# Optimization experiments

Hardware: AMD Instinct MI355X
Metric: run time of the kernel (lower is better)

The kernel has to match this reference:

```python
import jax, jax.numpy as jnp
import numpy as np

EPS = 1e-5

def convbn_relu(x, W, g, b, m, v):
    # 1x1 conv [O,C] on NCHW input, then inference-mode BN, then ReLU
    y = jnp.einsum('oc,bchw->bohw', W, x)
    scale = (g * jax.lax.rsqrt(v + EPS))[:, None, None]
    y = (y - m[:, None, None]) * scale + b[:, None, None]
    return jax.nn.relu(y)


def setup_inputs() -> dict:
    key = jax.random.key(0)
    ks = jax.random.split(key, 7)
    B, C, H, W = 2, 256, 96, 96
    L = 6  # psi1, psi2, phi1, phi2, f_down, f_up
    x = jax.random.normal(ks[0], (B, C, H, W), dtype=jnp.float32)
    f_k = jax.random.normal(ks[1], (B, C, H, W), dtype=jnp.float32)
    Ws = jax.random.normal(ks[2], (L, C, C), dtype=jnp.float32) * (1.0 / 16.0)
    gammas = jax.random.uniform(ks[3], (L, C), dtype=jnp.float32)
    betas = jax.random.normal(ks[4], (L, C), dtype=jnp.float32) * 0.1
    means = jax.random.normal(ks[5], (L, C), dtype=jnp.float32) * 0.1
    vars_ = jax.random.uniform(ks[6], (L, C), dtype=jnp.float32) + 0.5
    return {"x": x, "f_k": f_k, "Ws": Ws, "gammas": gammas, "betas": betas, "means": means, "vars_": vars_}


def reference(x, f_k, Ws, gammas, betas, means, vars_):
    B, C, H, W = x.shape
    K = Ws.shape[1]
    p = lambda i: (Ws[i], gammas[i], betas[i], means[i], vars_[i])
    # psi(x): two convbn+relu
    q = convbn_relu(convbn_relu(x, *p(0)), *p(1)).reshape(B, K, H * W)
    q = jnp.transpose(q, (0, 2, 1))                      # [B, N, K]
    # phi(f_k): two convbn+relu
    k = convbn_relu(convbn_relu(f_k, *p(2)), *p(3)).reshape(B, K, H * W)  # [B, K, N]
    # f_down(f_k)
    v = convbn_relu(f_k, *p(4)).reshape(B, K, H * W)
    v = jnp.transpose(v, (0, 2, 1))                      # [B, N, K]
    # attention WITHOUT 1/sqrt(d) scaling, as in the original
    sim = jnp.einsum('bnk,bkm->bnm', q, k)               # [B, N, N]
    sim = jax.nn.softmax(sim, axis=-1)
    ctx = jnp.einsum('bnm,bmk->bnk', sim, v)             # [B, N, K]
    ctx = jnp.transpose(ctx, (0, 2, 1)).reshape(B, K, H, W)
    # f_up
    return convbn_relu(ctx, *p(5))
```

## Files before the change

kernel.cpp:

```cpp
#include <hip/hip_runtime.h>
#include <hip/hip_bf16.h>

typedef __bf16 bf16;
typedef __bf16 bf16x8 __attribute__((ext_vector_type(8)));
typedef float floatx4 __attribute__((ext_vector_type(4)));
typedef float floatx16 __attribute__((ext_vector_type(16)));

#define MFMA_BF16(a, b, c) __builtin_amdgcn_mfma_f32_16x16x32_bf16((a), (b), (c), 0, 0, 0)
#define MFMA32(a, b, c) __builtin_amdgcn_mfma_f32_32x32x16_bf16((a), (b), (c), 0, 0, 0)

static constexpr int CH = 256;
static constexpr int NPIX = 9216;
static constexpr int MTOT = 2 * NPIX;
static constexpr int NQB2 = 144;

__device__ __forceinline__ void async16(void* lds, const void* g) {
  __builtin_amdgcn_global_load_lds(
      (const __attribute__((address_space(1))) void*)g,
      (__attribute__((address_space(3))) void*)lds, 16, 0, 0);
}

__device__ __forceinline__ unsigned cvtpk(float lo, float hi) {
  unsigned r;
  asm("v_cvt_pk_bf16_f32 %0, %1, %2" : "=v"(r) : "v"(lo), "v"(hi));
  return r;
}

__device__ __forceinline__ void plswap(unsigned& a, unsigned& b) {
  asm volatile("v_permlane32_swap_b32 %0, %1" : "+v"(a), "+v"(b));
}
__device__ __forceinline__ float xmax32(float v) {
  unsigned a = __builtin_bit_cast(unsigned, v), b = a;
  plswap(a, b);
  return fmaxf(__builtin_bit_cast(float, a), __builtin_bit_cast(float, b));
}
__device__ __forceinline__ float xsum32(float v) {
  unsigned a = __builtin_bit_cast(unsigned, v), b = a;
  plswap(a, b);
  return __builtin_bit_cast(float, a) + __builtin_bit_cast(float, b);
}

__global__ void split_transpose2(const float* __restrict__ xin, const float* __restrict__ fkin,
                                 bf16* __restrict__ ohx, bf16* __restrict__ olx,
                                 bf16* __restrict__ ohf, bf16* __restrict__ olf,
                                 const float* __restrict__ W,
                                 const float* __restrict__ g, const float* __restrict__ b,
                                 const float* __restrict__ m, const float* __restrict__ v,
                                 bf16* __restrict__ Wh, bf16* __restrict__ Wl,
                                 float* __restrict__ scale, float* __restrict__ bias) {
  __shared__ float t[64][65];
  int bid = blockIdx.x;
  int tid = threadIdx.x;

  {
    int i = bid * 256 + tid;
    if (i < 6 * CH * CH) {
      float wv = W[i];
      bf16 h = (bf16)wv;
      Wh[i] = h;
      Wl[i] = (bf16)(wv - (float)h);
    }
    if (i < 6 * CH) {
      float s = g[i] * rsqrtf(v[i] + 1e-5f);
      scale[i] = s;
      bias[i] = b[i] - m[i] * s;
    }
  }

  const float* in; bf16 *oh, *ol;
  if (bid >= 1152) { in = fkin; oh = ohf; ol = olf; bid -= 1152; }
  else             { in = xin;  oh = ohx; ol = olx; }
  int bb = bid / 576, rem = bid % 576;
  int ct = rem / 144, nt = rem % 144;
  int c0 = ct * 64, n0 = nt * 64;
  int cr = tid >> 4, nc = (tid & 15) * 4;
  for (int rr = 0; rr < 64; rr += 16) {
    int c = cr + rr;
    const float* p = in + ((size_t)(bb * CH + c0 + c) * NPIX) + n0 + nc;
    float4 val = *(const float4*)p;
    t[c][nc + 0] = val.x; t[c][nc + 1] = val.y;
    t[c][nc + 2] = val.z; t[c][nc + 3] = val.w;
  }
  __syncthreads();
  int n = tid >> 2, cb = (tid & 3) * 16;
  bf16 hb[16], lb[16];
#pragma unroll
  for (int j = 0; j < 16; j++) {
    float xv = t[cb + j][n];
    bf16 h = (bf16)xv;
    hb[j] = h;
    lb[j] = (bf16)(xv - (float)h);
  }
  size_t idx = (size_t)(bb * NPIX + n0 + n) * CH + c0 + cb;
  *(bf16x8*)&oh[idx]     = *(bf16x8*)&hb[0];
  *(bf16x8*)&oh[idx + 8] = *(bf16x8*)&hb[8];
  *(bf16x8*)&ol[idx]     = *(bf16x8*)&lb[0];
  *(bf16x8*)&ol[idx + 8] = *(bf16x8*)&lb[8];
}

struct ConvJob {
  const bf16 *Ah, *Al, *Bh, *Bl;
  const float *scale, *bias;
  bf16 *Yh, *Yl; float *Yf;
  int mode;
  int bid0;
};

__global__ __launch_bounds__(256, 3) void conv128(ConvJob j0, ConvJob j1, ConvJob j2) {
  __shared__ bf16 lds[4][8 * 512];
  int gbid = blockIdx.x;
  ConvJob j; int bid;
  if (gbid < 288)      { j = j0; bid = gbid; }
  else if (gbid < 576) { j = j1; bid = gbid - 288; }
  else                 { j = j2; bid = gbid - 576 + j2.bid0; }

  int tid = threadIdx.x;
  int w = tid >> 6, l = tid & 63;
  int q = l >> 4, c16 = l & 15;
  int m0 = (bid >> 1) * 128;
  int o0 = (bid & 1) * 128;

  const bf16* src = (w == 0) ? j.Ah : (w == 1) ? j.Al : (w == 2) ? j.Bh : j.Bl;
  int rowbase = (w < 2) ? m0 : o0;
  const bf16* gp = src + (size_t)(rowbase + c16) * CH + q * 8;
  bf16* ldst = &lds[w][0];

  const floatx4 zero4 = {0.f, 0.f, 0.f, 0.f};
  floatx4 acc[4][4];
#pragma unroll
  for (int i = 0; i < 4; i++)
#pragma unroll
    for (int jj = 0; jj < 4; jj++) acc[i][jj] = zero4;

  int mo16 = (w & 1) * 4, no16 = (w >> 1) * 4;

  for (int k0 = 0; k0 < CH; k0 += 32) {
#pragma unroll
    for (int f = 0; f < 8; f++)
      async16(ldst + f * 512, gp + (size_t)f * 16 * CH + k0);
    __syncthreads();

    bf16x8 ah[4], al[4], bh[4], bl[4];
#pragma unroll
    for (int i = 0; i < 4; i++) {
      ah[i] = *(const bf16x8*)&lds[0][(mo16 + i) * 512 + l * 8];
      al[i] = *(const bf16x8*)&lds[1][(mo16 + i) * 512 + l * 8];
      bh[i] = *(const bf16x8*)&lds[2][(no16 + i) * 512 + l * 8];
      bl[i] = *(const bf16x8*)&lds[3][(no16 + i) * 512 + l * 8];
    }
#pragma unroll
    for (int i = 0; i < 4; i++)
#pragma unroll
      for (int jj = 0; jj < 4; jj++) {
        acc[i][jj] = MFMA_BF16(ah[i], bh[jj], acc[i][jj]);
        acc[i][jj] = MFMA_BF16(ah[i], bl[jj], acc[i][jj]);
        acc[i][jj] = MFMA_BF16(al[i], bh[jj], acc[i][jj]);
      }
    __syncthreads();
  }

  int mo = (w & 1) * 64, no = (w >> 1) * 64;
  float sc[4], bs[4];
#pragma unroll
  for (int jj = 0; jj < 4; jj++) {
    int o = o0 + no + 16 * jj + c16;
    sc[jj] = j.scale[o];
    bs[jj] = j.bias[o];
  }

  if (j.mode == 3) {
    bf16* tile = &lds[0][0];
    int b2 = (m0 >= NPIX) ? 1 : 0;
    int nr0 = m0 - b2 * NPIX;
#pragma unroll
    for (int hc = 0; hc < 2; hc++) {
      __syncthreads();
      if ((w >> 1) == hc) {
#pragma unroll
        for (int i = 0; i < 4; i++)
#pragma unroll
          for (int jj = 0; jj < 4; jj++)
#pragma unroll
            for (int r = 0; r < 4; r++) {
              float y = acc[i][jj][r] * sc[jj] + bs[jj];
              y = fmaxf(y, 0.f);
              int chl = no + 16 * jj + c16 - hc * 64;
              int rowl = mo + 16 * i + 4 * q + r;
              tile[chl * 136 + rowl] = (bf16)y;
            }
      }
      __syncthreads();
      int chl = tid >> 2, rseg = (tid & 3) * 32;
      bf16* dst = j.Yh + ((size_t)(b2 * CH + o0 + hc * 64 + chl)) * NPIX + nr0 + rseg;
#pragma unroll
      for (int k = 0; k < 4; k++)
        *(bf16x8*)(dst + 8 * k) = *(bf16x8*)&tile[chl * 136 + rseg + 8 * k];
    }
    return;
  }

#pragma unroll
  for (int i = 0; i < 4; i++) {
    int nrow = m0 + mo + 16 * i + 4 * q;
#pragma unroll
    for (int jj = 0; jj < 4; jj++) {
      int o = o0 + no + 16 * jj + c16;
#pragma unroll
      for (int r = 0; r < 4; r++) {
        float y = acc[i][jj][r] * sc[jj] + bs[jj];
        y = fmaxf(y, 0.f);
        size_t idx = (size_t)(nrow + r) * CH + o;
        if (j.mode == 2) {
          j.Yf[idx] = y;
        } else if (j.mode == 1) {
          j.Yh[idx] = (bf16)y;
        } else {
          bf16 h = (bf16)y;
          j.Yh[idx] = h;
          j.Yl[idx] = (bf16)(y - (float)h);
        }
      }
    }
  }
}

__global__ __launch_bounds__(256, 4) void conv64(
    const bf16* __restrict__ Ah, const bf16* __restrict__ Al,
    const bf16* __restrict__ Bh, const bf16* __restrict__ Bl,
    const float* __restrict__ scale, const float* __restrict__ bias,
    float* __restrict__ Yf) {
  __shared__ bf16 lds[24 * 512];
  int tid = threadIdx.x;
  int w = tid >> 6, l = tid & 63;
  int q = l >> 4, c16 = l & 15;
  int m0 = (blockIdx.x >> 1) * 64;
  int o0 = (blockIdx.x & 1) * 128;

  const floatx4 zero4 = {0.f, 0.f, 0.f, 0.f};
  floatx4 acc[4][2];
#pragma unroll
  for (int i = 0; i < 4; i++) { acc[i][0] = zero4; acc[i][1] = zero4; }

  for (int k0 = 0; k0 < CH; k0 += 32) {
#pragma unroll
    for (int ff = 0; ff < 6; ff++) {
      int f = w * 6 + ff;
      const bf16* src; int rbase, fl;
      if (f < 4)       { src = Ah; rbase = m0; fl = f; }
      else if (f < 8)  { src = Al; rbase = m0; fl = f - 4; }
      else if (f < 16) { src = Bh; rbase = o0; fl = f - 8; }
      else             { src = Bl; rbase = o0; fl = f - 16; }
      async16(&lds[f * 512], src + (size_t)(rbase + fl * 16 + c16) * CH + k0 + q * 8);
    }
    __syncthreads();

    bf16x8 ah[4], al[4], bh[2], bl[2];
#pragma unroll
    for (int i = 0; i < 4; i++) {
      ah[i] = *(const bf16x8*)&lds[(0 + i) * 512 + l * 8];
      al[i] = *(const bf16x8*)&lds[(4 + i) * 512 + l * 8];
    }
#pragma unroll
    for (int n = 0; n < 2; n++) {
      bh[n] = *(const bf16x8*)&lds[(8 + 2 * w + n) * 512 + l * 8];
      bl[n] = *(const bf16x8*)&lds[(16 + 2 * w + n) * 512 + l * 8];
    }
#pragma unroll
    for (int i = 0; i < 4; i++)
#pragma unroll
      for (int n = 0; n < 2; n++) {
        acc[i][n] = MFMA_BF16(ah[i], bh[n], acc[i][n]);
        acc[i][n] = MFMA_BF16(ah[i], bl[n], acc[i][n]);
        acc[i][n] = MFMA_BF16(al[i], bh[n], acc[i][n]);
      }
    __syncthreads();
  }

  float sc[2], bs[2];
#pragma unroll
  for (int n = 0; n < 2; n++) {
    int o = o0 + 32 * w + 16 * n + c16;
    sc[n] = scale[o];
    bs[n] = bias[o];
  }

  float* tile = (float*)&lds[0];
  int b2 = (m0 >= NPIX) ? 1 : 0;
  int nr0 = m0 - b2 * NPIX;
#pragma unroll
  for (int hc = 0; hc < 2; hc++) {
    __syncthreads();
    if ((w >> 1) == hc) {
#pragma unroll
      for (int i = 0; i < 4; i++)
#pragma unroll
        for (int n = 0; n < 2; n++)
#pragma unroll
          for (int r = 0; r < 4; r++) {
            float y = acc[i][n][r] * sc[n] + bs[n];
            y = fmaxf(y, 0.f);
            int chl = 32 * (w - 2 * hc) + 16 * n + c16;
            int rowl = 16 * i + 4 * q + r;
            tile[chl * 68 + rowl] = y;
          }
    }
    __syncthreads();
    int chl = tid >> 2, rseg = (tid & 3) * 16;
    float* dst = Yf + ((size_t)(b2 * CH + o0 + hc * 64 + chl)) * NPIX + nr0 + rseg;
#pragma unroll
    for (int k = 0; k < 4; k++)
      *(float4*)(dst + 4 * k) = *(float4*)&tile[chl * 68 + rseg + 4 * k];
  }
}

__global__ __launch_bounds__(256, 2) void attn_part(
    const bf16* __restrict__ Q, const bf16* __restrict__ K, const bf16* __restrict__ Vt,
    float* __restrict__ Opart, float* __restrict__ Mpart, float* __restrict__ Lpart,
    int niter) {
  __shared__ bf16 lK[2][16 * 512];
  __shared__ bf16 lV[2][16 * 512];

  int tid = threadIdx.x;
  int w = tid >> 6, l = tid & 63;
  int ql = l & 31, hi = l >> 5;
  int bid = blockIdx.x;
  int qb = bid % NQB2, s = bid / NQB2;
  int b = qb / 72;
  int n0 = (qb % 72) * 128;
  int kv0 = s * niter * 32;
  size_t qkbase = (size_t)b * NPIX * CH;
  size_t vbase  = (size_t)b * CH * NPIX;

  bf16x8 qf[16];
  {
    const bf16* qp = Q + qkbase + (size_t)(n0 + 32 * w + ql) * CH + 8 * hi;
#pragma unroll
    for (int ks = 0; ks < 16; ks++) qf[ks] = *(const bf16x8*)(qp + ks * 16);
  }

  floatx16 oacc[8];
#pragma unroll
  for (int ct = 0; ct < 8; ct++)
#pragma unroll
    for (int r = 0; r < 16; r++) oacc[ct][r] = 0.f;
  float mrow = -1e30f, lrow = 0.f;

  const bf16* gK = K + qkbase + (size_t)kv0 * CH;
  const bf16* gV = Vt + vbase + kv0;

  auto stage = [&](int bi) {
#pragma unroll
    for (int ff = 0; ff < 4; ff++) {
      int f = 4 * w + ff;
      async16(&lK[bi][f * 512], gK + (size_t)ql * CH + f * 16 + 8 * hi);
      async16(&lV[bi][f * 512],
              gV + (size_t)((f >> 1) * 32 + ql) * NPIX + (f & 1) * 16 + 8 * hi);
    }
  };

  stage(0);

  for (int it = 0; it < niter; it++) {
    int cur = it & 1;
    __syncthreads();

    if (it + 1 < niter) {
      gK += 32 * CH; gV += 32;
      stage(cur ^ 1);
    }

    floatx16 sfA, sfB;
#pragma unroll
    for (int r = 0; r < 16; r++) { sfA[r] = 0.f; sfB[r] = 0.f; }
    __builtin_amdgcn_s_setprio(1);
#pragma unroll
    for (int ks = 0; ks < 16; ks += 2) {
      bf16x8 kf0 = *(const bf16x8*)&lK[cur][(ks + 0) * 512 + l * 8];
      bf16x8 kf1 = *(const bf16x8*)&lK[cur][(ks + 1) * 512 + l * 8];
      sfA = MFMA32(kf0, qf[ks + 0], sfA);
      sfB = MFMA32(kf1, qf[ks + 1], sfB);
    }
    __builtin_amdgcn_s_setprio(0);
    float pm = -1e30f;
#pragma unroll
    for (int r = 0; r < 16; r++) {
      float sv = sfA[r] + sfB[r];
      sfA[r] = sv;
      pm = fmaxf(pm, sv);
    }
    pm = xmax32(pm);

    bool need = pm > mrow + 8.f;
    if (__ballot((int)need) != 0ull) {
      float mn = fmaxf(mrow, pm);
      float alpha = __expf(mrow - mn);
      mrow = mn;
      lrow *= alpha;
      float arow[16];
#pragma unroll
      for (int r = 0; r < 16; r++)
        arow[r] = __shfl(alpha, (r & 3) + 8 * (r >> 2) + 4 * hi);
#pragma unroll
      for (int ct = 0; ct < 8; ct++)
#pragma unroll
        for (int r = 0; r < 16; r++) oacc[ct][r] *= arow[r];
    }

    float p[16];
    float rs = 0.f;
#pragma unroll
    for (int r = 0; r < 16; r++) {
      p[r] = __expf(sfA[r] - mrow);
      rs += p[r];
    }
    lrow += xsum32(rs);

    unsigned pk0 = cvtpk(p[0], p[1]),   pk1 = cvtpk(p[2], p[3]);
    unsigned pk2 = cvtpk(p[4], p[5]),   pk3 = cvtpk(p[6], p[7]);
    unsigned pk4 = cvtpk(p[8], p[9]),   pk5 = cvtpk(p[10], p[11]);
    unsigned pk6 = cvtpk(p[12], p[13]), pk7 = cvtpk(p[14], p[15]);
    plswap(pk0, pk2); plswap(pk1, pk3);
    plswap(pk4, pk6); plswap(pk5, pk7);
    uint4 u0, u1;
    u0.x = pk0; u0.y = pk1; u0.z = pk2; u0.w = pk3;
    u1.x = pk4; u1.y = pk5; u1.z = pk6; u1.w = pk7;
    bf16x8 pa0 = __builtin_bit_cast(bf16x8, u0);
    bf16x8 pa1 = __builtin_bit_cast(bf16x8, u1);

    __builtin_amdgcn_s_setprio(1);
#pragma unroll
    for (int ct = 0; ct < 8; ct++) {
      bf16x8 vb0 = *(const bf16x8*)&lV[cur][(2 * ct + 0) * 512 + l * 8];
      bf16x8 vb1 = *(const bf16x8*)&lV[cur][(2 * ct + 1) * 512 + l * 8];
      oacc[ct] = MFMA32(pa0, vb0, oacc[ct]);
      oacc[ct] = MFMA32(pa1, vb1, oacc[ct]);
    }
    __builtin_amdgcn_s_setprio(0);
  }

  if (hi == 0) {
    Mpart[(size_t)bid * 128 + 32 * w + ql] = mrow;
    Lpart[(size_t)bid * 128 + 32 * w + ql] = lrow;
  }
  float* Ob = Opart + (size_t)bid * 128 * CH;
#pragma unroll
  for (int ct = 0; ct < 8; ct++)
#pragma unroll
    for (int r = 0; r < 16; r++) {
      int row = 32 * w + (r & 3) + 8 * (r >> 2) + 4 * hi;
      Ob[(size_t)row * CH + 32 * ct + ql] = oacc[ct][r];
    }
}

__global__ __launch_bounds__(256) void attn_combine(
    const float* __restrict__ Opart, const float* __restrict__ Mpart,
    const float* __restrict__ Lpart,
    bf16* __restrict__ Oh, bf16* __restrict__ Ol, int S) {
  __shared__ float wgt[8][32];
  __shared__ float invl[32];
  int qb = blockIdx.x >> 2;
  int r0 = (blockIdx.x & 3) * 32;
  int t = threadIdx.x;
  if (t < 32) {
    int row = r0 + t;
    float m = -1e30f;
    for (int s = 0; s < S; s++)
      m = fmaxf(m, Mpart[(size_t)(s * NQB2 + qb) * 128 + row]);
    float lsum = 0.f;
    for (int s = 0; s < S; s++) {
      float wv = __expf(Mpart[(size_t)(s * NQB2 + qb) * 128 + row] - m);
      wgt[s][t] = wv;
      lsum += wv * Lpart[(size_t)(s * NQB2 + qb) * 128 + row];
    }
    invl[t] = 1.0f / lsum;
  }
  __syncthreads();
  int c = t;
  for (int rr = 0; rr < 32; rr++) {
    int row = r0 + rr;
    float acc = 0.f;
    for (int s = 0; s < S; s++)
      acc += wgt[s][rr] * Opart[((size_t)(s * NQB2 + qb) * 128 + row) * CH + c];
    float y = acc * invl[rr];
    size_t idx = (size_t)(qb * 128 + row) * CH + c;
    bf16 h = (bf16)y;
    Oh[idx] = h;
    Ol[idx] = (bf16)(y - (float)h);
  }
}

extern "C" void kernel_launch(void* const* d_in, const int* in_sizes, int n_in,
                              void* d_out, int out_size, void* d_ws, size_t ws_size,
                              hipStream_t stream) {
  const float* x  = (const float*)d_in[0];
  const float* fk = (const float*)d_in[1];
  const float* Ws = (const float*)d_in[2];
  const float* g  = (const float*)d_in[3];
  const float* be = (const float*)d_in[4];
  const float* me = (const float*)d_in[5];
  const float* va = (const float*)d_in[6];
  float* out = (float*)d_out;

  char* p = (char*)d_ws;
  bf16* Wh = (bf16*)p; p += (size_t)6 * CH * CH * 2;
  bf16* Wl = (bf16*)p; p += (size_t)6 * CH * CH * 2;
  float* scale = (float*)p; p += (size_t)6 * CH * 4;
  float* bias  = (float*)p; p += (size_t)6 * CH * 4;
  size_t plane = (size_t)MTOT * CH * 2;
  bf16* S0h = (bf16*)p; p += plane;
  bf16* S0l = (bf16*)p; p += plane;
  bf16* Qh  = (bf16*)p; p += plane;
  bf16* Kh  = (bf16*)p; p += plane;
  bf16* Vt  = (bf16*)p; p += plane;
  char* region = p;

  bf16* S2h = (bf16*)(region);
  bf16* S2l = (bf16*)(region + plane);
  bf16* P1h = (bf16*)(region + 2 * plane);
  bf16* P1l = (bf16*)(region + 3 * plane);
  bf16* F1h = (bf16*)(region + 4 * plane);
  bf16* F1l = (bf16*)(region + 5 * plane);

  size_t base_used = (size_t)(region - (char*)d_ws);
  size_t osz = (size_t)NQB2 * 128 * CH * 4;
  size_t per_split = osz + 2 * (size_t)NQB2 * 128 * 4;
  long avail = (long)ws_size - (long)base_used;
  int S = 1;
  {
    int cand[3] = {3, 2, 1};
    for (int i = 0; i < 3; i++)
      if ((long)cand[i] * (long)per_split <= avail) { S = cand[i]; break; }
  }
  float* Opart = (float*)region;
  float* Mpart = (float*)(region + (size_t)S * osz);
  float* Lpart = Mpart + (size_t)S * NQB2 * 128;

  (void)in_sizes; (void)n_in; (void)out_size;

  split_transpose2<<<2304, 256, 0, stream>>>(x, fk, S0h, S0l, S2h, S2l,
                                             Ws, g, be, me, va, Wh, Wl, scale, bias);

  auto W = [&](int layer) { return Wh + (size_t)layer * CH * CH; };
  auto Wlo = [&](int layer) { return Wl + (size_t)layer * CH * CH; };

  ConvJob psi1   {S0h, S0l, W(0), Wlo(0), scale + 0 * CH, bias + 0 * CH, P1h, P1l, nullptr, 0, 0};
  ConvJob phi1   {S2h, S2l, W(2), Wlo(2), scale + 2 * CH, bias + 2 * CH, F1h, F1l, nullptr, 0, 0};
  ConvJob fdownA {S2h, S2l, W(4), Wlo(4), scale + 4 * CH, bias + 4 * CH, Vt, nullptr, nullptr, 3, 0};
  ConvJob fdownB {S2h, S2l, W(4), Wlo(4), scale + 4 * CH, bias + 4 * CH, Vt, nullptr, nullptr, 3, 144};
  ConvJob psi2   {P1h, P1l, W(1), Wlo(1), scale + 1 * CH, bias + 1 * CH, Qh, nullptr, nullptr, 1, 0};
  ConvJob phi2   {F1h, F1l, W(3), Wlo(3), scale + 3 * CH, bias + 3 * CH, Kh, nullptr, nullptr, 1, 0};

  conv128<<<720, 256, 0, stream>>>(psi1, phi1, fdownA);
  conv128<<<720, 256, 0, stream>>>(psi2, phi2, fdownB);
  attn_part<<<NQB2 * S, 256, 0, stream>>>(Qh, Kh, Vt, Opart, Mpart, Lpart, 288 / S);
  attn_combine<<<NQB2 * 4, 256, 0, stream>>>(Opart, Mpart, Lpart, S0h, S0l, S);
  conv64<<<576, 256, 0, stream>>>(S0h, S0l, W(5), Wlo(5), scale + 5 * CH, bias + 5 * CH, out);
}
```

Baseline: 461.0 us.

## Fuse x transpose and bf16 split into psi1 conv tile loading

The psi1 convolution now reads fp32 NCHW x directly, transposing it through a shared-memory scratch tile and splitting it into bf16 hi/lo parts inside the conv128 K-loop. This removes the separate preprocessing pass over x, and with it one round-trip of hi/lo intermediates through global memory. The preprocessing kernel now only handles f_k and the weights, launching fewer blocks. In exchange, the psi1 blocks do synchronous loads and conversion work, plus an extra barrier, in their inner loop, and the added LDS scratch may lower occupancy for all conv128 blocks.

After: 449.7 us. -2.5%, faster.

```diff
diff --git a/kernel.cpp b/kernel.cpp
--- a/kernel.cpp
+++ b/kernel.cpp
@@ -40,14 +40,13 @@
   return __builtin_bit_cast(float, a) + __builtin_bit_cast(float, b);
 }
 
-__global__ void split_transpose2(const float* __restrict__ xin, const float* __restrict__ fkin,
-                                 bf16* __restrict__ ohx, bf16* __restrict__ olx,
-                                 bf16* __restrict__ ohf, bf16* __restrict__ olf,
-                                 const float* __restrict__ W,
-                                 const float* __restrict__ g, const float* __restrict__ b,
-                                 const float* __restrict__ m, const float* __restrict__ v,
-                                 bf16* __restrict__ Wh, bf16* __restrict__ Wl,
-                                 float* __restrict__ scale, float* __restrict__ bias) {
+__global__ void split_fk(const float* __restrict__ fkin,
+                         bf16* __restrict__ ohf, bf16* __restrict__ olf,
+                         const float* __restrict__ W,
+                         const float* __restrict__ g, const float* __restrict__ b,
+                         const float* __restrict__ m, const float* __restrict__ v,
+                         bf16* __restrict__ Wh, bf16* __restrict__ Wl,
+                         float* __restrict__ scale, float* __restrict__ bias) {
   __shared__ float t[64][65];
   int bid = blockIdx.x;
   int tid = threadIdx.x;
@@ -66,17 +65,15 @@
       bias[i] = b[i] - m[i] * s;
     }
   }
-
-  const float* in; bf16 *oh, *ol;
-  if (bid >= 1152) { in = fkin; oh = ohf; ol = olf; bid -= 1152; }
-  else             { in = xin;  oh = ohx; ol = olx; }
+  if (bid >= 1152) return;
+
   int bb = bid / 576, rem = bid % 576;
   int ct = rem / 144, nt = rem % 144;
   int c0 = ct * 64, n0 = nt * 64;
   int cr = tid >> 4, nc = (tid & 15) * 4;
   for (int rr = 0; rr < 64; rr += 16) {
     int c = cr + rr;
-    const float* p = in + ((size_t)(bb * CH + c0 + c) * NPIX) + n0 + nc;
+    const float* p = fkin + ((size_t)(bb * CH + c0 + c) * NPIX) + n0 + nc;
     float4 val = *(const float4*)p;
     t[c][nc + 0] = val.x; t[c][nc + 1] = val.y;
     t[c][nc + 2] = val.z; t[c][nc + 3] = val.w;
@@ -92,10 +89,10 @@
     lb[j] = (bf16)(xv - (float)h);
   }
   size_t idx = (size_t)(bb * NPIX + n0 + n) * CH + c0 + cb;
-  *(bf16x8*)&oh[idx]     = *(bf16x8*)&hb[0];
-  *(bf16x8*)&oh[idx + 8] = *(bf16x8*)&hb[8];
-  *(bf16x8*)&ol[idx]     = *(bf16x8*)&lb[0];
-  *(bf16x8*)&ol[idx + 8] = *(bf16x8*)&lb[8];
+  *(bf16x8*)&ohf[idx]     = *(bf16x8*)&hb[0];
+  *(bf16x8*)&ohf[idx + 8] = *(bf16x8*)&hb[8];
+  *(bf16x8*)&olf[idx]     = *(bf16x8*)&lb[0];
+  *(bf16x8*)&olf[idx + 8] = *(bf16x8*)&lb[8];
 }
 
 struct ConvJob {
@@ -108,6 +105,7 @@
 
 __global__ __launch_bounds__(256, 3) void conv128(ConvJob j0, ConvJob j1, ConvJob j2) {
   __shared__ bf16 lds[4][8 * 512];
+  __shared__ float scr[32][132];
   int gbid = blockIdx.x;
   ConvJob j; int bid;
   if (gbid < 288)      { j = j0; bid = gbid; }
@@ -133,11 +131,52 @@
     for (int jj = 0; jj < 4; jj++) acc[i][jj] = zero4;
 
   int mo16 = (w & 1) * 4, no16 = (w >> 1) * 4;
+  bool m4 = (j.mode == 4);
+  const float* xsrc = (const float*)j.Ah;
+  int b2m = (m0 >= NPIX) ? 1 : 0;
+  int nr0m = m0 - b2m * NPIX;
 
   for (int k0 = 0; k0 < CH; k0 += 32) {
-#pragma unroll
-    for (int f = 0; f < 8; f++)
-      async16(ldst + f * 512, gp + (size_t)f * 16 * CH + k0);
+    if (m4) {
+      if (w >= 2) {
+#pragma unroll
+        for (int f = 0; f < 8; f++)
+          async16(ldst + f * 512, gp + (size_t)f * 16 * CH + k0);
+      }
+      {
+        const float* xp = xsrc + ((size_t)(b2m * CH + k0 + (tid >> 3))) * NPIX
+                          + nr0m + (tid & 7) * 16;
+        float4 v0 = ((const float4*)xp)[0];
+        float4 v1 = ((const float4*)xp)[1];
+        float4 v2 = ((const float4*)xp)[2];
+        float4 v3 = ((const float4*)xp)[3];
+        float* srow = &scr[tid >> 3][(tid & 7) * 16];
+        *(float4*)(srow + 0) = v0;  *(float4*)(srow + 4) = v1;
+        *(float4*)(srow + 8) = v2;  *(float4*)(srow + 12) = v3;
+      }
+      __syncthreads();
+#pragma unroll
+      for (int half = 0; half < 2; half++) {
+        int f = tid >> 5;
+        int l2 = (tid & 31) + half * 32;
+        int qq = l2 >> 4, cc = l2 & 15;
+        int row = f * 16 + cc;
+        bf16 hb[8], lb[8];
+#pragma unroll
+        for (int jj2 = 0; jj2 < 8; jj2++) {
+          float xv = scr[qq * 8 + jj2][row];
+          bf16 h = (bf16)xv;
+          hb[jj2] = h;
+          lb[jj2] = (bf16)(xv - (float)h);
+        }
+        *(bf16x8*)&lds[0][f * 512 + l2 * 8] = *(bf16x8*)&hb[0];
+        *(bf16x8*)&lds[1][f * 512 + l2 * 8] = *(bf16x8*)&lb[0];
+      }
+    } else {
+#pragma unroll
+      for (int f = 0; f < 8; f++)
+        async16(ldst + f * 512, gp + (size_t)f * 16 * CH + k0);
+    }
     __syncthreads();
 
     bf16x8 ah[4], al[4], bh[4], bl[4];
@@ -210,9 +249,7 @@
         float y = acc[i][jj][r] * sc[jj] + bs[jj];
         y = fmaxf(y, 0.f);
         size_t idx = (size_t)(nrow + r) * CH + o;
-        if (j.mode == 2) {
-          j.Yf[idx] = y;
-        } else if (j.mode == 1) {
+        if (j.mode == 1) {
           j.Yh[idx] = (bf16)y;
         } else {
           bf16 h = (bf16)y;
@@ -537,13 +574,13 @@
 
   (void)in_sizes; (void)n_in; (void)out_size;
 
-  split_transpose2<<<2304, 256, 0, stream>>>(x, fk, S0h, S0l, S2h, S2l,
-                                             Ws, g, be, me, va, Wh, Wl, scale, bias);
+  split_fk<<<1536, 256, 0, stream>>>(fk, S2h, S2l,
+                                     Ws, g, be, me, va, Wh, Wl, scale, bias);
 
   auto W = [&](int layer) { return Wh + (size_t)layer * CH * CH; };
   auto Wlo = [&](int layer) { return Wl + (size_t)layer * CH * CH; };
 
-  ConvJob psi1   {S0h, S0l, W(0), Wlo(0), scale + 0 * CH, bias + 0 * CH, P1h, P1l, nullptr, 0, 0};
+  ConvJob psi1   {(const bf16*)x, nullptr, W(0), Wlo(0), scale + 0 * CH, bias + 0 * CH, P1h, P1l, nullptr, 4, 0};
   ConvJob phi1   {S2h, S2l, W(2), Wlo(2), scale + 2 * CH, bias + 2 * CH, F1h, F1l, nullptr, 0, 0};
   ConvJob fdownA {S2h, S2l, W(4), Wlo(4), scale + 4 * CH, bias + 4 * CH, Vt, nullptr, nullptr, 3, 0};
   ConvJob fdownB {S2h, S2l, W(4), Wlo(4), scale + 4 * CH, bias + 4 * CH, Vt, nullptr, nullptr, 3, 144};
```
